# Optimization experiments

Hardware: AMD Instinct MI355X
Metric: run time of the kernel (lower is better)

The kernel has to match this reference:

```python
import jax, jax.numpy as jnp
import numpy as np

B, S, D, H = 2, 2048, 768, 12
DH = D // H  # 64


def setup_inputs() -> dict:
    key = jax.random.key(0)
    ks = jax.random.split(key, 8)
    std = 1.0 / np.sqrt(D)
    return {
        "q": jax.random.normal(ks[0], (B, S, D), dtype=jnp.float32),
        "k": jax.random.normal(ks[1], (B, S, D), dtype=jnp.float32),
        "v": jax.random.normal(ks[2], (B, S, D), dtype=jnp.float32),
        "Wq": jax.random.normal(ks[3], (D, D), dtype=jnp.float32) * std,
        "bq": jnp.zeros((D,), dtype=jnp.float32),
        "Wk": jax.random.normal(ks[4], (D, D), dtype=jnp.float32) * std,
        "bk": jnp.zeros((D,), dtype=jnp.float32),
        "Wv": jax.random.normal(ks[5], (D, D), dtype=jnp.float32) * std,
        "bv": jnp.zeros((D,), dtype=jnp.float32),
        "Wo": jax.random.normal(ks[6], (D, D), dtype=jnp.float32) * std,
        "bo": jnp.zeros((D,), dtype=jnp.float32),
    }


def reference(q, k, v, Wq, bq, Wk, bk, Wv, bv, Wo, bo):
    b, s, d = q.shape
    # linear projections then split heads: [b, s, d] -> [b, h, s, dh]
    def split(x):
        return x.reshape(b, s, H, DH).transpose(0, 2, 1, 3)

    qh = split(q @ Wq + bq)
    kh = split(k @ Wk + bk)
    vh = split(v @ Wv + bv)

    scale = 1.0 / jnp.sqrt(jnp.asarray(DH, dtype=q.dtype))
    # full [b, h, s, s] score matrix (faithful to the original unfused op)
    scores = jnp.einsum("bhqd,bhkd->bhqk", qh, kh) * scale
    # look-ahead mask: 1 above the diagonal, added as mask * -1e9
    look_ahead = jnp.triu(jnp.ones((s, s), dtype=scores.dtype), k=1)
    scores = scores + look_ahead * (-1e9)

    attn = jax.nn.softmax(scores, axis=-1)  # dropout is identity at inference
    ctx = jnp.einsum("bhqk,bhkd->bhqd", attn, vh)
    ctx = ctx.transpose(0, 2, 1, 3).reshape(b, s, d)
    return ctx @ Wo + bo
```

## Files before the change

kernel.cpp:

```cpp
#include <hip/hip_runtime.h>
#include <hip/hip_bf16.h>
#include <stdint.h>

#define Bz 2
#define Sz 2048
#define Dz 768
#define Hz 12
#define DHz 64
#define Mz (Bz*Sz)
#define NQT2 64

typedef __attribute__((ext_vector_type(4))) float f32x4;
typedef __attribute__((ext_vector_type(8))) short bf16x8;
typedef unsigned short u16;
typedef __attribute__((ext_vector_type(8))) unsigned short u16x8;

__device__ __forceinline__ u16 f2bf(float f) {
  union { float f; uint32_t u; } c; c.f = f;
  uint32_t u = c.u;
  return (u16)((u + 0x7fffu + ((u >> 16) & 1u)) >> 16);
}

#define GLL16(gsrc, ldst) \
  __builtin_amdgcn_global_load_lds((const __attribute__((address_space(1))) void*)(gsrc), \
                                   (__attribute__((address_space(3))) void*)(ldst), 16, 0, 0)

__device__ __forceinline__ f32x4 mfma16(bf16x8 a, bf16x8 b, f32x4 c) {
  return __builtin_amdgcn_mfma_f32_16x16x32_bf16(a, b, c, 0, 0, 0);
}

__global__ void cvt3_kernel(const float* __restrict__ qa, const float* __restrict__ ka,
                            const float* __restrict__ va,
                            u16* __restrict__ qo, u16* __restrict__ ko, u16* __restrict__ vo,
                            int n8) {
  int i = blockIdx.x * blockDim.x + threadIdx.x;
  if (i >= n8) return;
  int z = blockIdx.y;
  const float* src = (z == 0) ? qa : (z == 1) ? ka : va;
  u16* dst = (z == 0) ? qo : (z == 1) ? ko : vo;
  const float4* s4 = (const float4*)src;
  float4 a = s4[(size_t)i * 2];
  float4 b = s4[(size_t)i * 2 + 1];
  u16x8 o;
  o[0] = f2bf(a.x); o[1] = f2bf(a.y); o[2] = f2bf(a.z); o[3] = f2bf(a.w);
  o[4] = f2bf(b.x); o[5] = f2bf(b.y); o[6] = f2bf(b.z); o[7] = f2bf(b.w);
  *(u16x8*)(dst + (size_t)i * 8) = o;
}

__global__ void wtrans4_kernel(const float* __restrict__ W0, const float* __restrict__ W1,
                               const float* __restrict__ W2, const float* __restrict__ W3,
                               u16* __restrict__ T0, u16* __restrict__ T1,
                               u16* __restrict__ T2, u16* __restrict__ T3) {
  __shared__ float tile[32][33];
  int z = blockIdx.z;
  const float* W = (z == 0) ? W0 : (z == 1) ? W1 : (z == 2) ? W2 : W3;
  u16* Wt = (z == 0) ? T0 : (z == 1) ? T1 : (z == 2) ? T2 : T3;
  int bx = blockIdx.x * 32, by = blockIdx.y * 32;
  int tx = threadIdx.x & 31, ty = threadIdx.x >> 5;
#pragma unroll
  for (int i = 0; i < 32; i += 8)
    tile[ty + i][tx] = W[(size_t)(by + ty + i) * Dz + bx + tx];
  __syncthreads();
#pragma unroll
  for (int i = 0; i < 32; i += 8)
    Wt[(size_t)(bx + ty + i) * Dz + by + tx] = f2bf(tile[tx][ty + i]);
}

__device__ __forceinline__ void gemm_core(
    const u16* __restrict__ A, const u16* __restrict__ Wt,
    const float* __restrict__ bias, void* __restrict__ out, int mode, float oscale,
    u16* As, u16* Bs)
{
  const int tid = threadIdx.x;
  const int wid = tid >> 6, lane = tid & 63;
  const int wm = wid >> 1, wn = wid & 1;
  const int m0 = blockIdx.x * 128, n0 = blockIdx.y * 128;
  const int fq = lane >> 4, fr = lane & 15;

  int aoff[2];
#pragma unroll
  for (int c = 0; c < 2; ++c) {
    int off  = (wid * 2 + c) * 1024 + lane * 16;
    int row  = off >> 6;
    int colb = (off & 63) ^ (((row >> 1) & 3) << 4);
    aoff[c]  = row * Dz + (colb >> 1);
  }

  int raddr[4], rbaddr[4];
#pragma unroll
  for (int f = 0; f < 4; ++f) {
    int rowA = wm * 64 + f * 16 + fr;
    raddr[f]  = rowA * 64 + ((fq * 16) ^ (((rowA >> 1) & 3) << 4));
    int rowB = wn * 64 + f * 16 + fr;
    rbaddr[f] = rowB * 64 + ((fq * 16) ^ (((rowB >> 1) & 3) << 4));
  }

  f32x4 acc[4][4];
  const f32x4 zero = {0.f, 0.f, 0.f, 0.f};
#pragma unroll
  for (int i = 0; i < 4; ++i)
#pragma unroll
    for (int j = 0; j < 4; ++j) acc[i][j] = zero;

  const u16* Abase = A + (size_t)m0 * Dz;
  const u16* Bbase = Wt + (size_t)n0 * Dz;

  for (int kt = 0; kt < Dz; kt += 32) {
#pragma unroll
    for (int c = 0; c < 2; ++c) {
      GLL16(Abase + kt + aoff[c], (char*)As + (wid * 2 + c) * 1024);
      GLL16(Bbase + kt + aoff[c], (char*)Bs + (wid * 2 + c) * 1024);
    }
    __syncthreads();
    bf16x8 af[4], bf[4];
#pragma unroll
    for (int f = 0; f < 4; ++f) {
      af[f] = *(const bf16x8*)((const char*)As + raddr[f]);
      bf[f] = *(const bf16x8*)((const char*)Bs + rbaddr[f]);
    }
    __builtin_amdgcn_s_setprio(1);
#pragma unroll
    for (int i = 0; i < 4; ++i)
#pragma unroll
      for (int j = 0; j < 4; ++j)
        acc[i][j] = mfma16(af[i], bf[j], acc[i][j]);
    __builtin_amdgcn_s_setprio(0);
    __syncthreads();
  }

  if (mode == 2) {
    float* O = (float*)out;
#pragma unroll
    for (int i = 0; i < 4; ++i) {
      int grow = m0 + wm * 64 + i * 16 + fq * 4;
#pragma unroll
      for (int j = 0; j < 4; ++j) {
        int gcol = n0 + wn * 64 + j * 16 + fr;
        float bv = bias[gcol];
#pragma unroll
        for (int r = 0; r < 4; ++r)
          O[(size_t)(grow + r) * Dz + gcol] = acc[i][j][r] + bv;
      }
    }
  } else {
    u16* O = (u16*)out;
#pragma unroll
    for (int i = 0; i < 4; ++i) {
      int grow = m0 + wm * 64 + i * 16 + fq * 4;
#pragma unroll
      for (int j = 0; j < 4; ++j) {
        int gcol = n0 + wn * 64 + j * 16 + fr;
        float bv = bias[gcol];
        int h = gcol >> 6, dh = gcol & 63;
#pragma unroll
        for (int r = 0; r < 4; ++r) {
          int t = grow + r;
          int b = t >> 11, s = t & 2047;
          float v = (acc[i][j][r] + bv) * oscale;
          if (mode == 0)
            O[((size_t)(b * Hz + h) * Sz + s) * DHz + dh] = f2bf(v);
          else
            O[((size_t)(b * Hz + h) * DHz + dh) * Sz + s] = f2bf(v);
        }
      }
    }
  }
}

#define QSCALE 0.1803368801111404f

__global__ __launch_bounds__(256, 2) void gemm_qkv(
    const u16* __restrict__ qb, const u16* __restrict__ kb, const u16* __restrict__ vb,
    const u16* __restrict__ Wqt, const u16* __restrict__ Wkt, const u16* __restrict__ Wvt,
    const float* __restrict__ bq, const float* __restrict__ bk, const float* __restrict__ bv,
    u16* __restrict__ Qh, u16* __restrict__ Kh, u16* __restrict__ Vt)
{
  __shared__ u16 As[128 * 32];
  __shared__ u16 Bs[128 * 32];
  const u16* A; const u16* W; const float* bias; u16* out; int mode; float osc;
  if (blockIdx.z == 0)      { A = qb; W = Wqt; bias = bq; out = Qh; mode = 0; osc = QSCALE; }
  else if (blockIdx.z == 1) { A = kb; W = Wkt; bias = bk; out = Kh; mode = 0; osc = 1.f; }
  else                      { A = vb; W = Wvt; bias = bv; out = Vt; mode = 1; osc = 1.f; }
  gemm_core(A, W, bias, out, mode, osc, As, Bs);
}

__global__ __launch_bounds__(256, 2) void gemm_out_k(
    const u16* __restrict__ ctx, const u16* __restrict__ Wot,
    const float* __restrict__ bo, float* __restrict__ out)
{
  __shared__ u16 As[128 * 32];
  __shared__ u16 Bs[128 * 32];
  gemm_core(ctx, Wot, bo, (void*)out, 2, 1.f, As, Bs);
}

__device__ __forceinline__ void stage_kv(const u16* __restrict__ Kg, const u16* __restrict__ Vg,
                                         int kt, u16* Ks, u16* Vs, int wid, int lane) {
#pragma unroll
  for (int c = 0; c < 4; ++c) {
    int off  = (wid * 4 + c) * 1024 + lane * 16;
    int row  = off >> 7;
    int colb = (off & 127) ^ ((row & 7) << 4);
    GLL16(Kg + ((size_t)(kt * 64 + row)) * DHz + (colb >> 1), (char*)Ks + (wid * 4 + c) * 1024);
    GLL16(Vg + (size_t)row * Sz + kt * 64 + (colb >> 1),      (char*)Vs + (wid * 4 + c) * 1024);
  }
}

__device__ __forceinline__ void attn_group(
    const bf16x8* aq, const bf16x8 kfr[4][2], const bf16x8 vfr[4][2],
    f32x4* o, float* m_r, float* l_r, char* Pw,
    int qbase, int kt, bool diag, int fq, int fr)
{
  const f32x4 zero = {0.f, 0.f, 0.f, 0.f};
  f32x4 s[4];
#pragma unroll
  for (int j = 0; j < 4; ++j) s[j] = zero;
  __builtin_amdgcn_s_setprio(1);
#pragma unroll
  for (int j = 0; j < 4; ++j)
#pragma unroll
    for (int kk = 0; kk < 2; ++kk)
      s[j] = mfma16(aq[kk], kfr[j][kk], s[j]);
  __builtin_amdgcn_s_setprio(0);

  if (diag) {
#pragma unroll
    for (int j = 0; j < 4; ++j) {
      int keyg = kt * 64 + j * 16 + fr;
#pragma unroll
      for (int r = 0; r < 4; ++r)
        if (keyg > qbase + fq * 4 + r) s[j][r] = -1e30f;
    }
  }

  float mt[4];
#pragma unroll
  for (int r = 0; r < 4; ++r) mt[r] = s[0][r];
#pragma unroll
  for (int j = 1; j < 4; ++j)
#pragma unroll
    for (int r = 0; r < 4; ++r) mt[r] = fmaxf(mt[r], s[j][r]);

  int nd = 0;
#pragma unroll
  for (int r = 0; r < 4; ++r) nd |= (mt[r] > m_r[r] + 8.f) ? 1 : 0;
  if (__any(nd)) {
#pragma unroll
    for (int msk = 1; msk < 16; msk <<= 1)
#pragma unroll
      for (int r = 0; r < 4; ++r) mt[r] = fmaxf(mt[r], __shfl_xor(mt[r], msk));
#pragma unroll
    for (int r = 0; r < 4; ++r) {
      float mn = fmaxf(m_r[r], mt[r]);
      float alpha = __builtin_amdgcn_exp2f(m_r[r] - mn);
      m_r[r] = mn;
      l_r[r] *= alpha;
#pragma unroll
      for (int i = 0; i < 4; ++i) o[i][r] *= alpha;
    }
  }

#pragma unroll
  for (int j = 0; j < 4; ++j) {
#pragma unroll
    for (int r = 0; r < 4; ++r) {
      float e = __builtin_amdgcn_exp2f(s[j][r] - m_r[r]);
      l_r[r] += e;
      int qr = fq * 4 + r;
      int key2 = (j * 16 + fr) * 2;
      *(u16*)(Pw + qr * 128 + (key2 ^ ((qr & 7) << 4))) = f2bf(e);
    }
  }

  __builtin_amdgcn_s_setprio(1);
#pragma unroll
  for (int kk = 0; kk < 2; ++kk) {
    int cbP = (kk * 64 + fq * 16) ^ ((fr & 7) << 4);
    bf16x8 pa = *(const bf16x8*)(Pw + fr * 128 + cbP);
#pragma unroll
    for (int fo = 0; fo < 4; ++fo)
      o[fo] = mfma16(pa, vfr[fo][kk], o[fo]);
  }
  __builtin_amdgcn_s_setprio(0);
}

__global__ __launch_bounds__(128, 2) void attn_kernel(
    const u16* __restrict__ Qh, const u16* __restrict__ Kh,
    const u16* __restrict__ Vt, u16* __restrict__ ctx)
{
  __shared__ u16 Ks[2][64 * 64];
  __shared__ u16 Vs[2][64 * 64];
  __shared__ u16 Ps[2 * 16 * 64];
  const int tid = threadIdx.x, wid = tid >> 6, lane = tid & 63;
  const int fq = lane >> 4, fr = lane & 15;
  const int bh = blockIdx.x;
  const int p = blockIdx.y;
  const int b = bh / Hz, h = bh % Hz;
  const int qb0 = p * 32 + wid * 16;
  const int qb1 = (NQT2 - 1 - p) * 32 + wid * 16;
  const int nkt = ((NQT2 - p) * 32 + 63) / 64;
  const int nlo = ((p + 1) * 32 + 63) / 64;

  const u16* Kg = Kh + (size_t)bh * Sz * DHz;
  const u16* Vg = Vt + (size_t)bh * DHz * Sz;
  const u16* Qg = Qh + (size_t)bh * Sz * DHz;

  bf16x8 aq[2][2];
#pragma unroll
  for (int kk = 0; kk < 2; ++kk) {
    aq[0][kk] = *(const bf16x8*)(Qg + (qb0 + fr) * DHz + kk * 32 + fq * 8);
    aq[1][kk] = *(const bf16x8*)(Qg + (qb1 + fr) * DHz + kk * 32 + fq * 8);
  }

  const f32x4 zero = {0.f, 0.f, 0.f, 0.f};
  f32x4 o[2][4];
#pragma unroll
  for (int g = 0; g < 2; ++g)
#pragma unroll
    for (int i = 0; i < 4; ++i) o[g][i] = zero;
  float m_r[2][4], l_r[2][4];
#pragma unroll
  for (int g = 0; g < 2; ++g)
#pragma unroll
    for (int r = 0; r < 4; ++r) { m_r[g][r] = -1e30f; l_r[g][r] = 0.f; }

  char* Pw = (char*)(Ps + wid * 16 * 64);

  stage_kv(Kg, Vg, 0, Ks[0], Vs[0], wid, lane);
  int cur = 0;

  for (int kt = 0; kt < nkt; ++kt) {
    __syncthreads();
    if (kt + 1 < nkt)
      stage_kv(Kg, Vg, kt + 1, Ks[cur ^ 1], Vs[cur ^ 1], wid, lane);

    const char* Kb = (const char*)Ks[cur];
    const char* Vb = (const char*)Vs[cur];

    bf16x8 kfr[4][2];
#pragma unroll
    for (int j = 0; j < 4; ++j) {
      int rowK = j * 16 + fr;
#pragma unroll
      for (int kk = 0; kk < 2; ++kk)
        kfr[j][kk] = *(const bf16x8*)(Kb + rowK * 128 + ((kk * 64 + fq * 16) ^ ((rowK & 7) << 4)));
    }
    bf16x8 vfr[4][2];
#pragma unroll
    for (int fo = 0; fo < 4; ++fo) {
      int rowV = fo * 16 + fr;
#pragma unroll
      for (int kk = 0; kk < 2; ++kk)
        vfr[fo][kk] = *(const bf16x8*)(Vb + rowV * 128 + ((kk * 64 + fq * 16) ^ ((rowV & 7) << 4)));
    }

    if (kt < nlo)
      attn_group(aq[0], kfr, vfr, o[0], m_r[0], l_r[0], Pw, qb0, kt, kt == nlo - 1, fq, fr);
    attn_group(aq[1], kfr, vfr, o[1], m_r[1], l_r[1], Pw, qb1, kt, kt == nkt - 1, fq, fr);

    cur ^= 1;
  }

#pragma unroll
  for (int msk = 1; msk < 16; msk <<= 1)
#pragma unroll
    for (int g = 0; g < 2; ++g)
#pragma unroll
      for (int r = 0; r < 4; ++r) l_r[g][r] += __shfl_xor(l_r[g][r], msk);

#pragma unroll
  for (int g = 0; g < 2; ++g) {
    int qb = (g == 0) ? qb0 : qb1;
#pragma unroll
    for (int fo = 0; fo < 4; ++fo) {
      int dh = fo * 16 + fr;
#pragma unroll
      for (int r = 0; r < 4; ++r) {
        int qg = qb + fq * 4 + r;
        ctx[((size_t)b * Sz + qg) * Dz + h * DHz + dh] = f2bf(o[g][fo][r] / l_r[g][r]);
      }
    }
  }
}

extern "C" void kernel_launch(void* const* d_in, const int* in_sizes, int n_in,
                              void* d_out, int out_size, void* d_ws, size_t ws_size,
                              hipStream_t stream) {
  const float* q  = (const float*)d_in[0];
  const float* k  = (const float*)d_in[1];
  const float* v  = (const float*)d_in[2];
  const float* Wq = (const float*)d_in[3];
  const float* bq = (const float*)d_in[4];
  const float* Wk = (const float*)d_in[5];
  const float* bk = (const float*)d_in[6];
  const float* Wv = (const float*)d_in[7];
  const float* bv = (const float*)d_in[8];
  const float* Wo = (const float*)d_in[9];
  const float* bo = (const float*)d_in[10];
  float* out = (float*)d_out;

  char* ws = (char*)d_ws;
  size_t off = 0;
  auto alloc = [&](size_t bytes) {
    void* p = ws + off;
    off += (bytes + 255) & ~(size_t)255;
    return p;
  };
  u16* qb  = (u16*)alloc((size_t)Mz * Dz * 2);
  u16* kb  = (u16*)alloc((size_t)Mz * Dz * 2);
  u16* vb  = (u16*)alloc((size_t)Mz * Dz * 2);
  u16* Wqt = (u16*)alloc((size_t)Dz * Dz * 2);
  u16* Wkt = (u16*)alloc((size_t)Dz * Dz * 2);
  u16* Wvt = (u16*)alloc((size_t)Dz * Dz * 2);
  u16* Wot = (u16*)alloc((size_t)Dz * Dz * 2);
  u16* Qh  = (u16*)alloc((size_t)Bz * Hz * Sz * DHz * 2);
  u16* Kh  = (u16*)alloc((size_t)Bz * Hz * Sz * DHz * 2);
  u16* Vtr = (u16*)alloc((size_t)Bz * Hz * DHz * Sz * 2);
  u16* ctx = (u16*)alloc((size_t)Mz * Dz * 2);

  int n8 = Mz * Dz / 8;
  int cblk = (n8 + 255) / 256;
  cvt3_kernel<<<dim3(cblk, 3), 256, 0, stream>>>(q, k, v, qb, kb, vb, n8);

  wtrans4_kernel<<<dim3(Dz / 32, Dz / 32, 4), 256, 0, stream>>>(
      Wq, Wk, Wv, Wo, Wqt, Wkt, Wvt, Wot);

  gemm_qkv<<<dim3(Mz / 128, Dz / 128, 3), 256, 0, stream>>>(
      qb, kb, vb, Wqt, Wkt, Wvt, bq, bk, bv, Qh, Kh, Vtr);

  attn_kernel<<<dim3(Bz * Hz, NQT2 / 2), 128, 0, stream>>>(Qh, Kh, Vtr, ctx);

  gemm_out_k<<<dim3(Mz / 128, Dz / 128), 256, 0, stream>>>(ctx, Wot, bo, out);
}
```

Before: 106.0 us.

## Triple-buffer LDS tiles with partial vmcnt waits in GEMM and attention loops

Both GEMM kernels move from a single LDS buffer, which needed two barriers per k-step, to a three-stage ring. Each step prefetches the next tile and waits only for the older loads with a partial vmcnt count, then uses one barrier. The attention kernel's K/V staging goes from double to triple buffering in the same way, dropping the wait-for-everything sync. This aims to overlap global-to-LDS loads with MFMA work at the cost of more LDS per block, which could lower occupancy, and it depends on the hand-written vmcnt counts being correct.

```diff
diff --git a/kernel.cpp b/kernel.cpp
--- a/kernel.cpp
+++ b/kernel.cpp
@@ -69,7 +69,7 @@
 __device__ __forceinline__ void gemm_core(
     const u16* __restrict__ A, const u16* __restrict__ Wt,
     const float* __restrict__ bias, void* __restrict__ out, int mode, float oscale,
-    u16* As, u16* Bs)
+    u16 (*As)[128 * 32], u16 (*Bs)[128 * 32])
 {
   const int tid = threadIdx.x;
   const int wid = tid >> 6, lane = tid & 63;
@@ -105,18 +105,35 @@
   const u16* Abase = A + (size_t)m0 * Dz;
   const u16* Bbase = Wt + (size_t)n0 * Dz;
 
-  for (int kt = 0; kt < Dz; kt += 32) {
-#pragma unroll
-    for (int c = 0; c < 2; ++c) {
-      GLL16(Abase + kt + aoff[c], (char*)As + (wid * 2 + c) * 1024);
-      GLL16(Bbase + kt + aoff[c], (char*)Bs + (wid * 2 + c) * 1024);
-    }
-    __syncthreads();
+  const int NKT = Dz / 32;
+#pragma unroll
+  for (int c = 0; c < 2; ++c) {
+    GLL16(Abase + aoff[c], (char*)As[0] + (wid * 2 + c) * 1024);
+    GLL16(Bbase + aoff[c], (char*)Bs[0] + (wid * 2 + c) * 1024);
+  }
+  int cur = 0;
+
+  for (int kt = 0; kt < NKT; ++kt) {
+    int nx = cur + 1; if (nx == 3) nx = 0;
+    if (kt + 1 < NKT) {
+      int ke = (kt + 1) * 32;
+#pragma unroll
+      for (int c = 0; c < 2; ++c) {
+        GLL16(Abase + ke + aoff[c], (char*)As[nx] + (wid * 2 + c) * 1024);
+        GLL16(Bbase + ke + aoff[c], (char*)Bs[nx] + (wid * 2 + c) * 1024);
+      }
+      asm volatile("s_waitcnt vmcnt(4)" ::: "memory");
+    } else {
+      asm volatile("s_waitcnt vmcnt(0)" ::: "memory");
+    }
+    __builtin_amdgcn_s_barrier();
+    __builtin_amdgcn_sched_barrier(0);
+
     bf16x8 af[4], bf[4];
 #pragma unroll
     for (int f = 0; f < 4; ++f) {
-      af[f] = *(const bf16x8*)((const char*)As + raddr[f]);
-      bf[f] = *(const bf16x8*)((const char*)Bs + rbaddr[f]);
+      af[f] = *(const bf16x8*)((const char*)As[cur] + raddr[f]);
+      bf[f] = *(const bf16x8*)((const char*)Bs[cur] + rbaddr[f]);
     }
     __builtin_amdgcn_s_setprio(1);
 #pragma unroll
@@ -125,7 +142,7 @@
       for (int j = 0; j < 4; ++j)
         acc[i][j] = mfma16(af[i], bf[j], acc[i][j]);
     __builtin_amdgcn_s_setprio(0);
-    __syncthreads();
+    cur = nx;
   }
 
   if (mode == 2) {
@@ -175,8 +192,8 @@
     const float* __restrict__ bq, const float* __restrict__ bk, const float* __restrict__ bv,
     u16* __restrict__ Qh, u16* __restrict__ Kh, u16* __restrict__ Vt)
 {
-  __shared__ u16 As[128 * 32];
-  __shared__ u16 Bs[128 * 32];
+  __shared__ u16 As[3][128 * 32];
+  __shared__ u16 Bs[3][128 * 32];
   const u16* A; const u16* W; const float* bias; u16* out; int mode; float osc;
   if (blockIdx.z == 0)      { A = qb; W = Wqt; bias = bq; out = Qh; mode = 0; osc = QSCALE; }
   else if (blockIdx.z == 1) { A = kb; W = Wkt; bias = bk; out = Kh; mode = 0; osc = 1.f; }
@@ -188,8 +205,8 @@
     const u16* __restrict__ ctx, const u16* __restrict__ Wot,
     const float* __restrict__ bo, float* __restrict__ out)
 {
-  __shared__ u16 As[128 * 32];
-  __shared__ u16 Bs[128 * 32];
+  __shared__ u16 As[3][128 * 32];
+  __shared__ u16 Bs[3][128 * 32];
   gemm_core(ctx, Wot, bo, (void*)out, 2, 1.f, As, Bs);
 }
 
@@ -287,8 +304,8 @@
     const u16* __restrict__ Qh, const u16* __restrict__ Kh,
     const u16* __restrict__ Vt, u16* __restrict__ ctx)
 {
-  __shared__ u16 Ks[2][64 * 64];
-  __shared__ u16 Vs[2][64 * 64];
+  __shared__ u16 Ks[3][64 * 64];
+  __shared__ u16 Vs[3][64 * 64];
   __shared__ u16 Ps[2 * 16 * 64];
   const int tid = threadIdx.x, wid = tid >> 6, lane = tid & 63;
   const int fq = lane >> 4, fr = lane & 15;
@@ -329,9 +346,15 @@
   int cur = 0;
 
   for (int kt = 0; kt < nkt; ++kt) {
-    __syncthreads();
-    if (kt + 1 < nkt)
-      stage_kv(Kg, Vg, kt + 1, Ks[cur ^ 1], Vs[cur ^ 1], wid, lane);
+    int nx = cur + 1; if (nx == 3) nx = 0;
+    if (kt + 1 < nkt) {
+      stage_kv(Kg, Vg, kt + 1, Ks[nx], Vs[nx], wid, lane);
+      asm volatile("s_waitcnt vmcnt(8)" ::: "memory");
+    } else {
+      asm volatile("s_waitcnt vmcnt(0)" ::: "memory");
+    }
+    __builtin_amdgcn_s_barrier();
+    __builtin_amdgcn_sched_barrier(0);
 
     const char* Kb = (const char*)Ks[cur];
     const char* Vb = (const char*)Vs[cur];
@@ -357,7 +380,7 @@
       attn_group(aq[0], kfr, vfr, o[0], m_r[0], l_r[0], Pw, qb0, kt, kt == nlo - 1, fq, fr);
     attn_group(aq[1], kfr, vfr, o[1], m_r[1], l_r[1], Pw, qb1, kt, kt == nkt - 1, fq, fr);
 
-    cur ^= 1;
+    cur = nx;
   }
 
 #pragma unroll
```

Result: no change. 104.3 us (-1.7%).
